# Optimization experiments

Hardware: AMD Instinct MI355X
Metric: run time of the kernel (lower is better)

The kernel has to match this reference:

```python
import jax, jax.numpy as jnp
import numpy as np

H = 1024        # hidden_size
NH = 16         # num_heads
HD = H // NH    # head_dim
DFF = 4 * H
SCALE = HD ** -0.5
EPS = 1e-5


def _ln(x, g, b):
    m = jnp.mean(x, axis=-1, keepdims=True)
    v = jnp.var(x, axis=-1, keepdims=True)
    return (x - m) * jax.lax.rsqrt(v + EPS) * g + b


def _heads(t, B):
    # [B, S, H] -> [B, NH, S, HD]
    return t.reshape(B, -1, NH, HD).transpose(0, 2, 1, 3)


def _merge(t, B):
    # [B, NH, S, HD] -> [B, S, H]
    return t.transpose(0, 2, 1, 3).reshape(B, -1, H)


def _attn(q, k, v):
    s = jnp.einsum('bhqd,bhkd->bhqk', q, k) * SCALE
    p = jax.nn.softmax(s, axis=-1)
    p = jnp.nan_to_num(p, nan=0.0)
    return jnp.einsum('bhqk,bhkd->bhqd', p, v)


def setup_inputs() -> dict:
    key = jax.random.key(0)
    ks = jax.random.split(key, 16)
    std = (2.0 / (5 * H)) ** 0.5
    B, S, SI = 2, 2048, 256
    d = {
        'x': jax.random.normal(ks[0], (B, S, H), jnp.float32),
        'image_features': jax.random.normal(ks[1], (B, SI, H), jnp.float32),
    }
    names = ['sq', 'sk', 'sv', 'so', 'cq', 'ck', 'cv', 'co']
    for i, n in enumerate(names):
        d['W_' + n] = std * jax.random.normal(ks[2 + i], (H, H), jnp.float32)
        d['b_' + n] = jnp.zeros((H,), jnp.float32)
    d['W_ff1'] = std * jax.random.normal(ks[10], (H, DFF), jnp.float32)
    d['b_ff1'] = jnp.zeros((DFF,), jnp.float32)
    d['W_ff2'] = std * jax.random.normal(ks[11], (DFF, H), jnp.float32)
    d['b_ff2'] = jnp.zeros((H,), jnp.float32)
    for n in ['ln1', 'ln2', 'ln3']:
        d['g_' + n] = jnp.ones((H,), jnp.float32)
        d['b_' + n] = jnp.zeros((H,), jnp.float32)
    return d


def reference(x, image_features,
              W_sq, b_sq, W_sk, b_sk, W_sv, b_sv, W_so, b_so,
              W_cq, b_cq, W_ck, b_ck, W_cv, b_cv, W_co, b_co,
              W_ff1, b_ff1, W_ff2, b_ff2,
              g_ln1, b_ln1, g_ln2, b_ln2, g_ln3, b_ln3):
    B = x.shape[0]
    x = x * 0.1
    img = image_features * 0.1

    # --- self attention (pre-norm) ---
    nx = _ln(x, g_ln1, b_ln1)
    q = _heads(nx @ W_sq + b_sq, B)
    k = _heads(nx @ W_sk + b_sk, B)
    v = _heads(nx @ W_sv + b_sv, B)
    so = _merge(_attn(q, k, v), B) @ W_so + b_so
    x = x + so

    # --- cross attention (pre-norm) ---
    nx = _ln(x, g_ln2, b_ln2)
    q = _heads(nx @ W_cq + b_cq, B)
    k = _heads(img @ W_ck + b_ck, B)
    v = _heads(img @ W_cv + b_cv, B)
    co = _merge(_attn(q, k, v), B) @ W_co + b_co
    x = x + co

    # --- feed forward (pre-norm) ---
    nx = _ln(x, g_ln3, b_ln3)
    ff = jax.nn.gelu(nx @ W_ff1 + b_ff1, approximate=False) @ W_ff2 + b_ff2
    x = x + ff
    return x * 10.0
```

## Files before the change

kernel.cpp:

```cpp
#include <hip/hip_runtime.h>
#include <hip/hip_bf16.h>

typedef __bf16 bf16;
typedef __bf16 bf16x4 __attribute__((ext_vector_type(4)));
typedef __bf16 bf16x8 __attribute__((ext_vector_type(8)));
typedef float  f32x4  __attribute__((ext_vector_type(4)));
typedef float  f32x16 __attribute__((ext_vector_type(16)));
typedef int    int4v  __attribute__((ext_vector_type(4)));

#define H_DIM 1024
#define NHEAD 16
#define HD    64
#define QSCL 0.18033688011112042f

__device__ __forceinline__ void gload_lds16(const bf16* g, bf16* l) {
    __builtin_amdgcn_global_load_lds((const __attribute__((address_space(1))) void*)g,
                                     (__attribute__((address_space(3))) void*)l, 16, 0, 0);
}
__device__ __forceinline__ void gload_lds16_u8(const unsigned char* g, unsigned char* l) {
    __builtin_amdgcn_global_load_lds((const __attribute__((address_space(1))) void*)g,
                                     (__attribute__((address_space(3))) void*)l, 16, 0, 0);
}

__device__ __forceinline__ unsigned cvtpk_bf16(float lo, float hi) {
    unsigned r;
    asm volatile("v_cvt_pk_bf16_f32 %0, %1, %2" : "=v"(r) : "v"(lo), "v"(hi));
    return r;
}
__device__ __forceinline__ unsigned cvt2_fp8(float a, float b) {
    unsigned r;
    asm volatile("v_cvt_pk_fp8_f32 %0, %1, %2" : "=v"(r) : "v"(a), "v"(b));
    return r & 0xffffu;
}
__device__ __forceinline__ unsigned pack4_fp8(float a, float b, float c, float d) {
    return cvt2_fp8(a, b) | (cvt2_fp8(c, d) << 16);
}

__device__ __forceinline__ float fexp2(float x) {
    float r;
    asm("v_exp_f32 %0, %1" : "=v"(r) : "v"(x));
    return r;
}

__device__ __forceinline__ void wconv_body(const float* __restrict__ W,
                                           bf16* __restrict__ Wt, int K, int N,
                                           int bx, int by, int t) {
    __shared__ float tile[64][65];
    const int n0 = bx * 64, k0 = by * 64;
#pragma unroll
    for (int p = 0; p < 4; ++p) {
        int lin = p * 1024 + t * 4;
        int r = lin >> 6, c = lin & 63;
        f32x4 v = *(const f32x4*)(W + (size_t)(k0 + r) * N + n0 + c);
        tile[r][c]     = v[0];
        tile[r][c + 1] = v[1];
        tile[r][c + 2] = v[2];
        tile[r][c + 3] = v[3];
    }
    __syncthreads();
#pragma unroll
    for (int p = 0; p < 4; ++p) {
        int lin = p * 1024 + t * 4;
        int rn = lin >> 6, ck = lin & 63;
        bf16x4 o;
#pragma unroll
        for (int j = 0; j < 4; ++j) o[j] = (bf16)tile[ck + j][rn];
        *(bf16x4*)(Wt + (size_t)(n0 + rn) * K + k0 + ck) = o;
    }
}

__global__ __launch_bounds__(256) void wconv_kernel(const float* __restrict__ W,
                                                    bf16* __restrict__ Wt,
                                                    int K, int N) {
    wconv_body(W, Wt, K, N, blockIdx.x, blockIdx.y, threadIdx.x);
}

struct WPtrs { const float* w[4]; bf16* o[4]; };
__global__ __launch_bounds__(256) void wconv4_kernel(WPtrs p) {
    const int m = blockIdx.z;
    wconv_body(p.w[m], p.o[m], 1024, 1024, blockIdx.x, blockIdx.y, threadIdx.x);
}

struct W3Ptrs { const float* w[3]; };
__global__ __launch_bounds__(256) void wconv_fp8_kernel(W3Ptrs p, unsigned char* __restrict__ out) {
    __shared__ float tile[64][65];
    const int m = blockIdx.z, t = threadIdx.x;
    const float* W = p.w[m];
    unsigned char* Wt = out + (size_t)m * 1024 * 1024;
    const int n0 = blockIdx.x * 64, k0 = blockIdx.y * 64;
#pragma unroll
    for (int pp = 0; pp < 4; ++pp) {
        int lin = pp * 1024 + t * 4;
        int r = lin >> 6, c = lin & 63;
        f32x4 v = *(const f32x4*)(W + (size_t)(k0 + r) * 1024 + n0 + c);
        tile[r][c]     = v[0];
        tile[r][c + 1] = v[1];
        tile[r][c + 2] = v[2];
        tile[r][c + 3] = v[3];
    }
    __syncthreads();
#pragma unroll
    for (int pp = 0; pp < 4; ++pp) {
        int lin = pp * 1024 + t * 4;
        int rn = lin >> 6, ck = lin & 63;
        unsigned u = pack4_fp8(tile[ck][rn], tile[ck + 1][rn], tile[ck + 2][rn], tile[ck + 3][rn]);
        *(unsigned*)&Wt[(size_t)(n0 + rn) * 1024 + k0 + ck] = u;
    }
}

__global__ __launch_bounds__(256) void wconv_fp8g(const float* __restrict__ W,
                                                  unsigned char* __restrict__ Wt, int N) {
    __shared__ float tile[64][65];
    const int t = threadIdx.x;
    const int n0 = blockIdx.x * 64, k0 = blockIdx.y * 64;
#pragma unroll
    for (int pp = 0; pp < 4; ++pp) {
        int lin = pp * 1024 + t * 4;
        int r = lin >> 6, c = lin & 63;
        f32x4 v = *(const f32x4*)(W + (size_t)(k0 + r) * N + n0 + c);
        tile[r][c]     = v[0];
        tile[r][c + 1] = v[1];
        tile[r][c + 2] = v[2];
        tile[r][c + 3] = v[3];
    }
    __syncthreads();
#pragma unroll
    for (int pp = 0; pp < 4; ++pp) {
        int lin = pp * 1024 + t * 4;
        int rn = lin >> 6, ck = lin & 63;
        unsigned u = pack4_fp8(tile[ck][rn], tile[ck + 1][rn], tile[ck + 2][rn], tile[ck + 3][rn]);
        *(unsigned*)&Wt[(size_t)(n0 + rn) * 1024 + k0 + ck] = u;
    }
}

__global__ __launch_bounds__(256) void ln_kernel(const float* __restrict__ in, float inScale,
                                                 const float* __restrict__ g,
                                                 const float* __restrict__ b,
                                                 bf16* __restrict__ out) {
    const int row = blockIdx.x, t = threadIdx.x;
    const float* p = in + (size_t)row * H_DIM;
    f32x4 v = *(const f32x4*)(p + t * 4);
    v *= inScale;
    float s1 = v[0] + v[1] + v[2] + v[3];
    float s2 = v[0] * v[0] + v[1] * v[1] + v[2] * v[2] + v[3] * v[3];
#pragma unroll
    for (int m = 1; m < 64; m <<= 1) {
        s1 += __shfl_xor(s1, m);
        s2 += __shfl_xor(s2, m);
    }
    __shared__ float red[8];
    const int wave = t >> 6;
    if ((t & 63) == 0) { red[wave * 2] = s1; red[wave * 2 + 1] = s2; }
    __syncthreads();
    s1 = red[0] + red[2] + red[4] + red[6];
    s2 = red[1] + red[3] + red[5] + red[7];
    float mean = s1 * (1.0f / H_DIM);
    float var  = s2 * (1.0f / H_DIM) - mean * mean;
    float inv  = rsqrtf(var + 1e-5f);
    f32x4 gg = *(const f32x4*)(g + t * 4);
    f32x4 bb = *(const f32x4*)(b + t * 4);
    bf16x4 o;
#pragma unroll
    for (int j = 0; j < 4; ++j) o[j] = (bf16)((v[j] - mean) * inv * gg[j] + bb[j]);
    *(bf16x4*)(out + (size_t)row * H_DIM + t * 4) = o;
}

__global__ __launch_bounds__(256) void ln_fp8_kernel(const float* __restrict__ in, float inScale,
                                                     const float* __restrict__ g,
                                                     const float* __restrict__ b,
                                                     unsigned* __restrict__ out) {
    const int row = blockIdx.x, t = threadIdx.x;
    const float* p = in + (size_t)row * H_DIM;
    f32x4 v = *(const f32x4*)(p + t * 4);
    v *= inScale;
    float s1 = v[0] + v[1] + v[2] + v[3];
    float s2 = v[0] * v[0] + v[1] * v[1] + v[2] * v[2] + v[3] * v[3];
#pragma unroll
    for (int m = 1; m < 64; m <<= 1) {
        s1 += __shfl_xor(s1, m);
        s2 += __shfl_xor(s2, m);
    }
    __shared__ float red[8];
    const int wave = t >> 6;
    if ((t & 63) == 0) { red[wave * 2] = s1; red[wave * 2 + 1] = s2; }
    __syncthreads();
    s1 = red[0] + red[2] + red[4] + red[6];
    s2 = red[1] + red[3] + red[5] + red[7];
    float mean = s1 * (1.0f / H_DIM);
    float var  = s2 * (1.0f / H_DIM) - mean * mean;
    float inv  = rsqrtf(var + 1e-5f);
    f32x4 gg = *(const f32x4*)(g + t * 4);
    f32x4 bb = *(const f32x4*)(b + t * 4);
    float y0 = (v[0] - mean) * inv * gg[0] + bb[0];
    float y1 = (v[1] - mean) * inv * gg[1] + bb[1];
    float y2 = (v[2] - mean) * inv * gg[2] + bb[2];
    float y3 = (v[3] - mean) * inv * gg[3] + bb[3];
    out[row * 256 + t] = pack4_fp8(y0, y1, y2, y3);
}

__global__ __launch_bounds__(256) void cvt_scale_kernel(const float* __restrict__ in,
                                                        bf16* __restrict__ out,
                                                        float s, int n4) {
    int i = blockIdx.x * 256 + threadIdx.x;
    if (i < n4) {
        f32x4 v = *(const f32x4*)(in + (size_t)i * 4);
        bf16x4 o;
#pragma unroll
        for (int j = 0; j < 4; ++j) o[j] = (bf16)(v[j] * s);
        *(bf16x4*)(out + (size_t)i * 4) = o;
    }
}

template <int BM, int BN, int MODE, bool OUT_BF16, bool GELU_EPI, bool HAS_RES>
__global__ __launch_bounds__(256) void gemm_kernel(const bf16* __restrict__ A,
                                                   const bf16* __restrict__ Bt,
                                                   const float* __restrict__ bias1,
                                                   const float* __restrict__ bias2,
                                                   const float* __restrict__ bias3,
                                                   const float* __restrict__ res,
                                                   void* __restrict__ o1, void* __restrict__ o2,
                                                   void* __restrict__ o3,
                                                   int M, int N, int K,
                                                   float resScale, float outScale, int slog2) {
    constexpr int CHUNKS = (BM + BN) / 32;
    constexpr int WRR = BM / 2, WCC = BN / 2;
    constexpr int MI = WRR / 16, NJ = WCC / 16;
    __shared__ bf16 SM[2][(BM + BN) * 64];
    const int nwg = gridDim.x * gridDim.y;
    const int dlin = blockIdx.y * gridDim.x + blockIdx.x;
    const int id = (dlin & 7) * (nwg >> 3) + (dlin >> 3);
    const int bx = id % gridDim.x, by = id / gridDim.x;
    const int m0 = by * BM, n0 = bx * BN;
    const int tid = threadIdx.x;
    const int wave = tid >> 6, lane = tid & 63;
    const int lr = lane & 15, lhi = lane >> 4;
    const int wr = wave >> 1, wc = wave & 1;
    const int sr = lane >> 3, sc8 = (lane & 7) * 8;
    const int sc8x = sc8 ^ (sr << 3);
    const int rxr = (lr & 7) << 3;

    f32x4 acc[MI][NJ] = {};

    auto stage = [&](int buf, int k0) {
#pragma unroll
        for (int p = 0; p < CHUNKS; ++p) {
            const int rr = p * 32 + wave * 8 + sr;
            bf16* l = &SM[buf][0] + p * 2048 + wave * 512;
            const bf16* g = (p < BM / 32)
                ? (A  + (size_t)(m0 + rr) * K + k0 + sc8x)
                : (Bt + (size_t)(n0 + rr - BM) * K + k0 + sc8x);
            gload_lds16(g, l);
        }
    };

    stage(0, 0);
    int buf = 0;
    for (int k0 = 0; k0 < K; k0 += 64) {
        const bool pre = (k0 + 64 < K);
        if (pre) {
            stage(buf ^ 1, k0 + 64);
            asm volatile("s_waitcnt vmcnt(%0)" :: "i"(CHUNKS) : "memory");
        } else {
            asm volatile("s_waitcnt vmcnt(0)" ::: "memory");
        }
        __builtin_amdgcn_sched_barrier(0);
        __builtin_amdgcn_s_barrier();
#pragma unroll
        for (int kk = 0; kk < 2; ++kk) {
            const int sa = (kk * 32 + lhi * 8) ^ rxr;
            bf16x8 af[MI], bfr[NJ];
#pragma unroll
            for (int i = 0; i < MI; ++i)
                af[i] = *(const bf16x8*)&SM[buf][(wr * WRR + i * 16 + lr) * 64 + sa];
#pragma unroll
            for (int j = 0; j < NJ; ++j)
                bfr[j] = *(const bf16x8*)&SM[buf][(BM + wc * WCC + j * 16 + lr) * 64 + sa];
#pragma unroll
            for (int i = 0; i < MI; ++i)
#pragma unroll
                for (int j = 0; j < NJ; ++j)
                    acc[i][j] = __builtin_amdgcn_mfma_f32_16x16x32_bf16(af[i], bfr[j], acc[i][j], 0, 0, 0);
        }
        __builtin_amdgcn_s_barrier();
        buf ^= 1;
    }

#pragma unroll
    for (int i = 0; i < MI; ++i) {
#pragma unroll
        for (int j = 0; j < NJ; ++j) {
            const int col = n0 + wc * WCC + j * 16 + lr;
            const int row0 = m0 + wr * WRR + i * 16 + lhi * 4;
            if (MODE == 0) {
                const float bv = bias1[col];
#pragma unroll
                for (int r = 0; r < 4; ++r) {
                    const int row = row0 + r;
                    const size_t idx = (size_t)row * N + col;
                    float v = acc[i][j][r] + bv;
                    if (HAS_RES) v += res[idx] * resScale;
                    if (GELU_EPI) v = 0.5f * v * (1.0f + erff(v * 0.70710678118654752f));
                    v *= outScale;
                    if (OUT_BF16) ((bf16*)o1)[idx] = (bf16)v;
                    else          ((float*)o1)[idx] = v;
                }
            } else {
                const int sec = col >> 10, cl = col & 1023;
                const bool isV = (sec == 1);
                const float bv = (sec == 0 ? bias1 : bias2)[cl];
                if (!isV) {
                    bf16* dst = (bf16*)o1;
#pragma unroll
                    for (int r = 0; r < 4; ++r)
                        dst[(size_t)(row0 + r) * H_DIM + cl] = (bf16)(acc[i][j][r] + bv);
                } else {
                    bf16* dst = (bf16*)o2;
                    const int S = 1 << slog2;
                    const int hI = cl >> 6, dI = cl & 63;
                    const int bI = row0 >> slog2, s0 = row0 & (S - 1);
                    bf16x4 ov;
#pragma unroll
                    for (int r = 0; r < 4; ++r) ov[r] = (bf16)(acc[i][j][r] + bv);
                    *(bf16x4*)(dst + ((size_t)((bI * NHEAD + hI) * HD + dI)) * S + s0) = ov;
                }
            }
        }
    }
}

__global__ __launch_bounds__(256) void gemm_qkv_fp8(const unsigned char* __restrict__ A8,
                                                    const unsigned char* __restrict__ B8,
                                                    const float* __restrict__ bias1,
                                                    const float* __restrict__ bias2,
                                                    const float* __restrict__ bias3,
                                                    bf16* __restrict__ Qo, bf16* __restrict__ Ko,
                                                    bf16* __restrict__ Vo) {
    constexpr int Kd = 1024;
    __shared__ unsigned char SM[2][256 * 64];
    const int nwg = gridDim.x * gridDim.y;
    const int dlin = blockIdx.y * gridDim.x + blockIdx.x;
    const int id = (dlin & 7) * (nwg >> 3) + (dlin >> 3);
    const int bx = id % gridDim.x, by = id / gridDim.x;
    const int m0 = by * 128, n0 = bx * 128;
    const int tid = threadIdx.x;
    const int wave = tid >> 6, lane = tid & 63;
    const int l31 = lane & 31, l5 = lane >> 5;
    const int wr = wave >> 1, wc = wave & 1;
    const int srow = wave * 16 + (lane >> 2);
    const int sunit = (((lane & 3) ^ ((srow >> 1) & 3)) << 4);
    const int rxc = (l31 >> 1) & 3;

    f32x16 acc[2][2] = {};

    auto stage = [&](int buf, int k0) {
#pragma unroll
        for (int p = 0; p < 4; ++p) {
            const int rr = p * 64 + srow;
            unsigned char* l = &SM[buf][0] + p * 4096 + wave * 1024;
            const unsigned char* g = (p < 2)
                ? (A8 + (size_t)(m0 + rr) * Kd + k0 + sunit)
                : (B8 + (size_t)(n0 + rr - 128) * Kd + k0 + sunit);
            gload_lds16_u8(g, l);
        }
    };

    stage(0, 0);
    int buf = 0;
    for (int k0 = 0; k0 < Kd; k0 += 64) {
        const bool pre = (k0 + 64 < Kd);
        if (pre) {
            stage(buf ^ 1, k0 + 64);
            asm volatile("s_waitcnt vmcnt(4)" ::: "memory");
        } else {
            asm volatile("s_waitcnt vmcnt(0)" ::: "memory");
        }
        __builtin_amdgcn_sched_barrier(0);
        __builtin_amdgcn_s_barrier();
#pragma unroll
        for (int kk = 0; kk < 4; ++kk) {
            const int sa = (((kk ^ rxc) << 4) + l5 * 8);
            long long af[2], bfr[2];
#pragma unroll
            for (int i = 0; i < 2; ++i)
                af[i] = *(const long long*)&SM[buf][(wr * 64 + i * 32 + l31) * 64 + sa];
#pragma unroll
            for (int j = 0; j < 2; ++j)
                bfr[j] = *(const long long*)&SM[buf][(128 + wc * 64 + j * 32 + l31) * 64 + sa];
#pragma unroll
            for (int i = 0; i < 2; ++i)
#pragma unroll
                for (int j = 0; j < 2; ++j)
                    acc[i][j] = __builtin_amdgcn_mfma_f32_32x32x16_fp8_fp8(af[i], bfr[j], acc[i][j], 0, 0, 0);
        }
        __builtin_amdgcn_s_barrier();
        buf ^= 1;
    }

#pragma unroll
    for (int i = 0; i < 2; ++i) {
#pragma unroll
        for (int j = 0; j < 2; ++j) {
            const int col = n0 + wc * 64 + j * 32 + l31;
            const int rbase = m0 + wr * 64 + i * 32 + l5 * 4;
            const int sec = col >> 10, cl = col & 1023;
            const float bv = (sec == 0 ? bias1 : sec == 1 ? bias2 : bias3)[cl];
            if (sec < 2) {
                bf16* dst = (sec == 0) ? Qo : Ko;
                const float sc = (sec == 0) ? QSCL : 1.f;
#pragma unroll
                for (int rq = 0; rq < 4; ++rq)
#pragma unroll
                    for (int rr = 0; rr < 4; ++rr) {
                        const int row = rbase + rq * 8 + rr;
                        dst[(size_t)row * H_DIM + cl] = (bf16)((acc[i][j][rq * 4 + rr] + bv) * sc);
                    }
            } else {
                const int hI = cl >> 6, dI = cl & 63;
#pragma unroll
                for (int rq = 0; rq < 4; ++rq) {
                    const int row0 = rbase + rq * 8;
                    const int bI = row0 >> 11, s0 = row0 & 2047;
                    bf16x4 ov;
#pragma unroll
                    for (int rr = 0; rr < 4; ++rr) ov[rr] = (bf16)(acc[i][j][rq * 4 + rr] + bv);
                    *(bf16x4*)(Vo + ((size_t)((bI * NHEAD + hI) * HD + dI)) * 2048 + s0) = ov;
                }
            }
        }
    }
}

__global__ __launch_bounds__(256) void gemm_f8q(const unsigned char* __restrict__ A8,
                                                const unsigned char* __restrict__ B8,
                                                const float* __restrict__ bias,
                                                bf16* __restrict__ o1, int M, int NOUT) {
    constexpr int Kd = 1024;
    __shared__ unsigned char SM[2][256 * 64];
    const int nwg = gridDim.x * gridDim.y;
    const int dlin = blockIdx.y * gridDim.x + blockIdx.x;
    const int id = (dlin & 7) * (nwg >> 3) + (dlin >> 3);
    const int bx = id % gridDim.x, by = id / gridDim.x;
    const int m0 = by * 128, n0 = bx * 128;
    const int tid = threadIdx.x;
    const int wave = tid >> 6, lane = tid & 63;
    const int l31 = lane & 31, l5 = lane >> 5;
    const int wr = wave >> 1, wc = wave & 1;
    const int srow = wave * 16 + (lane >> 2);
    const int sunit = (((lane & 3) ^ ((srow >> 1) & 3)) << 4);
    const int rxc = (l31 >> 1) & 3;

    f32x16 acc[2][2] = {};

    auto stage = [&](int buf, int k0) {
#pragma unroll
        for (int p = 0; p < 4; ++p) {
            const int rr = p * 64 + srow;
            unsigned char* l = &SM[buf][0] + p * 4096 + wave * 1024;
            const unsigned char* g = (p < 2)
                ? (A8 + (size_t)(m0 + rr) * Kd + k0 + sunit)
                : (B8 + (size_t)(n0 + rr - 128) * Kd + k0 + sunit);
            gload_lds16_u8(g, l);
        }
    };

    stage(0, 0);
    int buf = 0;
    for (int k0 = 0; k0 < Kd; k0 += 64) {
        const bool pre = (k0 + 64 < Kd);
        if (pre) {
            stage(buf ^ 1, k0 + 64);
            asm volatile("s_waitcnt vmcnt(4)" ::: "memory");
        } else {
            asm volatile("s_waitcnt vmcnt(0)" ::: "memory");
        }
        __builtin_amdgcn_sched_barrier(0);
        __builtin_amdgcn_s_barrier();
#pragma unroll
        for (int kk = 0; kk < 4; ++kk) {
            const int sa = (((kk ^ rxc) << 4) + l5 * 8);
            long long af[2], bfr[2];
#pragma unroll
            for (int i = 0; i < 2; ++i)
                af[i] = *(const long long*)&SM[buf][(wr * 64 + i * 32 + l31) * 64 + sa];
#pragma unroll
            for (int j = 0; j < 2; ++j)
                bfr[j] = *(const long long*)&SM[buf][(128 + wc * 64 + j * 32 + l31) * 64 + sa];
#pragma unroll
            for (int i = 0; i < 2; ++i)
#pragma unroll
                for (int j = 0; j < 2; ++j)
                    acc[i][j] = __builtin_amdgcn_mfma_f32_32x32x16_fp8_fp8(af[i], bfr[j], acc[i][j], 0, 0, 0);
        }
        __builtin_amdgcn_s_barrier();
        buf ^= 1;
    }

#pragma unroll
    for (int i = 0; i < 2; ++i) {
#pragma unroll
        for (int j = 0; j < 2; ++j) {
            const int col = n0 + wc * 64 + j * 32 + l31;
            const int rbase = m0 + wr * 64 + i * 32 + l5 * 4;
            const float bv = bias[col];
#pragma unroll
            for (int rq = 0; rq < 4; ++rq)
#pragma unroll
                for (int rr = 0; rr < 4; ++rr) {
                    const int row = rbase + rq * 8 + rr;
                    o1[(size_t)row * NOUT + col] = (bf16)((acc[i][j][rq * 4 + rr] + bv) * QSCL);
                }
        }
    }
}

__global__ __launch_bounds__(256) void attn_kernel(const bf16* __restrict__ Qb,
                                                   const bf16* __restrict__ Kb,
                                                   const bf16* __restrict__ Vt_g,
                                                   bf16* __restrict__ Ob,
                                                   int SQ, int SK) {
    __shared__ bf16 SMEM[2][2][64 * 64];
    const int nwg = gridDim.x * gridDim.y;
    const int dlin = blockIdx.y * gridDim.x + blockIdx.x;
    const int id = (dlin & 7) * (nwg >> 3) + (dlin >> 3);
    const int NQ = gridDim.y;
    const int bh = id / NQ, qt = id - bh * NQ;
    const int b = bh >> 4, h = bh & 15;
    const int q0 = qt * 128;
    const int tid = threadIdx.x, wave = tid >> 6, lane = tid & 63;
    const int lr = lane & 15, lhi = lane >> 4;

    bf16x8 qf[2][2];
#pragma unroll
    for (int qi = 0; qi < 2; ++qi) {
        const bf16* qp = Qb + ((size_t)b * SQ + q0 + wave * 32 + qi * 16 + lr) * H_DIM + h * HD;
        qf[qi][0] = *(const bf16x8*)(qp + lhi * 8);
        qf[qi][1] = *(const bf16x8*)(qp + 32 + lhi * 8);
    }

    const int kx = (((lr & 3) | (((lr >> 2) & 1) << 2)) << 3);
    const int vx = (((lr & 3) | (((lr >> 3) & 1) << 2)) << 3);
    int krow[4];
#pragma unroll
    for (int nf = 0; nf < 4; ++nf)
        krow[nf] = (nf >> 1) * 32 + (lr >> 2) * 8 + (nf & 1) * 4 + (lr & 3);

    const int rS = tid >> 3, cS = (tid & 7) * 8;
    const int kxw = (((rS & 3) | (((rS >> 3) & 1) << 2)) << 3);
    const bf16* Kg = Kb + (size_t)b * SK * H_DIM + h * HD;
    const bf16* Vg = Vt_g + (size_t)bh * 64 * SK;

    bf16x8 onesv;
#pragma unroll
    for (int j = 0; j < 8; ++j) onesv[j] = (bf16)1.0f;

    f32x4 o[2][4] = {};
    f32x4 psum[2] = {};
    bf16x8 gK[2], gV[2];

    auto LOADG = [&](int kb) {
#pragma unroll
        for (int p = 0; p < 2; ++p) {
            gK[p] = *(const bf16x8*)(Kg + (size_t)(kb + p * 32 + rS) * H_DIM + cS);
            gV[p] = *(const bf16x8*)(Vg + (size_t)(p * 32 + rS) * SK + kb + cS);
        }
    };
    auto STORES = [&](int buf) {
#pragma unroll
        for (int p = 0; p < 2; ++p) {
            *(bf16x8*)&SMEM[buf][0][(p * 32 + rS) * 64 + (cS ^ kxw)] = gK[p];
            *(bf16x8*)&SMEM[buf][1][(p * 32 + rS) * 64 + (cS ^ kxw)] = gV[p];
        }
    };
    auto COMPUTE = [&](int buf) {
        f32x4 s[2][4] = {};
        __builtin_amdgcn_s_setprio(1);
#pragma unroll
        for (int nf = 0; nf < 4; ++nf) {
            const int base = krow[nf] * 64;
            bf16x8 kf0 = *(const bf16x8*)&SMEM[buf][0][base + ((lhi * 8) ^ kx)];
            bf16x8 kf1 = *(const bf16x8*)&SMEM[buf][0][base + ((32 + lhi * 8) ^ kx)];
#pragma unroll
            for (int qi = 0; qi < 2; ++qi) {
                s[qi][nf] = __builtin_amdgcn_mfma_f32_16x16x32_bf16(kf0, qf[qi][0], s[qi][nf], 0, 0, 0);
                s[qi][nf] = __builtin_amdgcn_mfma_f32_16x16x32_bf16(kf1, qf[qi][1], s[qi][nf], 0, 0, 0);
            }
        }
        __builtin_amdgcn_s_setprio(0);
        unsigned pw[2][8];
#pragma unroll
        for (int qi = 0; qi < 2; ++qi)
#pragma unroll
            for (int nf = 0; nf < 4; ++nf) {
                float p0 = fexp2(s[qi][nf][0]);
                float p1 = fexp2(s[qi][nf][1]);
                float p2 = fexp2(s[qi][nf][2]);
                float p3 = fexp2(s[qi][nf][3]);
                pw[qi][nf * 2]     = cvtpk_bf16(p0, p1);
                pw[qi][nf * 2 + 1] = cvtpk_bf16(p2, p3);
            }
        __builtin_amdgcn_s_setprio(1);
#pragma unroll
        for (int kk = 0; kk < 2; ++kk) {
            bf16x8 pb[2];
#pragma unroll
            for (int qi = 0; qi < 2; ++qi) {
                int4v w = { (int)pw[qi][kk * 4], (int)pw[qi][kk * 4 + 1],
                            (int)pw[qi][kk * 4 + 2], (int)pw[qi][kk * 4 + 3] };
                pb[qi] = __builtin_bit_cast(bf16x8, w);
                psum[qi] = __builtin_amdgcn_mfma_f32_16x16x32_bf16(onesv, pb[qi], psum[qi], 0, 0, 0);
            }
#pragma unroll
            for (int df = 0; df < 4; ++df) {
                bf16x8 vf = *(const bf16x8*)&SMEM[buf][1][(df * 16 + lr) * 64 + ((kk * 32 + lhi * 8) ^ vx)];
                o[0][df] = __builtin_amdgcn_mfma_f32_16x16x32_bf16(vf, pb[0], o[0][df], 0, 0, 0);
                o[1][df] = __builtin_amdgcn_mfma_f32_16x16x32_bf16(vf, pb[1], o[1][df], 0, 0, 0);
            }
        }
        __builtin_amdgcn_s_setprio(0);
    };

    const int nt = SK >> 6;
    LOADG(0);
    STORES(0);
    if (nt > 1) LOADG(64);
    __syncthreads();
    for (int t = 0; t < nt; ++t) {
        COMPUTE(t & 1);
        if (t + 1 < nt) {
            STORES((t + 1) & 1);
            if (t + 2 < nt) LOADG((t + 2) << 6);
        }
        __syncthreads();
    }

    bf16* T = &SMEM[0][0][0] + wave * (32 * 72);
#pragma unroll
    for (int qi = 0; qi < 2; ++qi) {
        const float inv = 1.0f / psum[qi][0];
#pragma unroll
        for (int df = 0; df < 4; ++df)
#pragma unroll
            for (int r = 0; r < 4; ++r)
                T[(qi * 16 + lr) * 72 + df * 16 + lhi * 4 + r] = (bf16)(o[qi][df][r] * inv);
    }
#pragma unroll
    for (int pp = 0; pp < 4; ++pp) {
        const int r32 = pp * 8 + (lane >> 3), ch = (lane & 7) * 8;
        bf16x8 v = *(const bf16x8*)&T[r32 * 72 + ch];
        *(bf16x8*)(Ob + ((size_t)b * SQ + q0 + wave * 32 + r32) * H_DIM + h * HD + ch) = v;
    }
}

extern "C" void kernel_launch(void* const* d_in, const int* in_sizes, int n_in,
                              void* d_out, int out_size, void* d_ws, size_t ws_size,
                              hipStream_t stream) {
    const float* x    = (const float*)d_in[0];
    const float* img  = (const float*)d_in[1];
    const float* W_sq = (const float*)d_in[2];   const float* b_sq = (const float*)d_in[3];
    const float* W_sk = (const float*)d_in[4];   const float* b_sk = (const float*)d_in[5];
    const float* W_sv = (const float*)d_in[6];   const float* b_sv = (const float*)d_in[7];
    const float* W_so = (const float*)d_in[8];   const float* b_so = (const float*)d_in[9];
    const float* W_cq = (const float*)d_in[10];  const float* b_cq = (const float*)d_in[11];
    const float* W_ck = (const float*)d_in[12];  const float* b_ck = (const float*)d_in[13];
    const float* W_cv = (const float*)d_in[14];  const float* b_cv = (const float*)d_in[15];
    const float* W_co = (const float*)d_in[16];  const float* b_co = (const float*)d_in[17];
    const float* W_f1 = (const float*)d_in[18];  const float* b_f1 = (const float*)d_in[19];
    const float* W_f2 = (const float*)d_in[20];  const float* b_f2 = (const float*)d_in[21];
    const float* g1 = (const float*)d_in[22];    const float* bb1 = (const float*)d_in[23];
    const float* g2 = (const float*)d_in[24];    const float* bb2 = (const float*)d_in[25];
    const float* g3 = (const float*)d_in[26];    const float* bb3 = (const float*)d_in[27];

    char* ws = (char*)d_ws;
    const size_t MB = 1ull << 20;
    unsigned char* LN2_8 = (unsigned char*)(ws + 0 * MB);
    unsigned char* wcq8  = (unsigned char*)(ws + 4 * MB);
    bf16* WT   = (bf16*)ws;
    bf16* w_so = WT + 3 * (1u << 20);
    bf16* w_ck = WT + 5 * (1u << 20);
    bf16* w_cv = WT + 6 * (1u << 20);
    bf16* w_co = WT + 7 * (1u << 20);
    bf16* w_f1 = WT + 8 * (1u << 20);
    bf16* w_f2 = WT + 12 * (1u << 20);
    float* XR  = (float*)(ws + 32 * MB);
    bf16* NX   = (bf16*)(ws + 48 * MB);
    bf16* Qb   = (bf16*)(ws + 56 * MB);
    bf16* Kb   = (bf16*)(ws + 64 * MB);
    bf16* Vt   = (bf16*)(ws + 72 * MB);
    bf16* FF   = (bf16*)(ws + 56 * MB);
    unsigned char* W8  = (unsigned char*)(ws + 80 * MB);
    unsigned char* NX8 = (unsigned char*)(ws + 83 * MB);
    bf16* IMGB = (bf16*)(ws + 88 * MB);

    const dim3 blk(256);

    WPtrs wp;
    wp.w[0] = W_so; wp.o[0] = w_so;  wp.w[1] = W_ck; wp.o[1] = w_ck;
    wp.w[2] = W_cv; wp.o[2] = w_cv;  wp.w[3] = W_co; wp.o[3] = w_co;
    wconv4_kernel<<<dim3(16, 16, 4), blk, 0, stream>>>(wp);
    W3Ptrs w3; w3.w[0] = W_sq; w3.w[1] = W_sk; w3.w[2] = W_sv;
    wconv_fp8_kernel<<<dim3(16, 16, 3), blk, 0, stream>>>(w3, W8);
    wconv_fp8g<<<dim3(16, 16), blk, 0, stream>>>(W_cq, wcq8, 1024);
    wconv_kernel<<<dim3(64, 16), blk, 0, stream>>>(W_f1, w_f1, 1024, 4096);
    wconv_kernel<<<dim3(16, 64), blk, 0, stream>>>(W_f2, w_f2, 4096, 1024);

    ln_fp8_kernel<<<4096, blk, 0, stream>>>(x, 0.1f, g1, bb1, (unsigned*)NX8);
    gemm_qkv_fp8<<<dim3(24, 32), blk, 0, stream>>>(NX8, W8, b_sq, b_sk, b_sv, Qb, Kb, Vt);
    attn_kernel<<<dim3(32, 16), blk, 0, stream>>>(Qb, Kb, Vt, NX, 2048, 2048);
    gemm_kernel<64, 128, 0, false, false, true><<<dim3(8, 64), blk, 0, stream>>>(
        NX, w_so, b_so, nullptr, nullptr, x, XR, nullptr, nullptr, 4096, 1024, 1024, 0.1f, 1.f, 0);

    ln_fp8_kernel<<<4096, blk, 0, stream>>>(XR, 1.f, g2, bb2, (unsigned*)LN2_8);
    gemm_f8q<<<dim3(8, 32), blk, 0, stream>>>(LN2_8, wcq8, b_cq, Qb, 4096, 1024);
    cvt_scale_kernel<<<dim3(512), blk, 0, stream>>>(img, IMGB, 0.1f, 131072);
    gemm_kernel<64, 128, 2, true, false, false><<<dim3(16, 8), blk, 0, stream>>>(
        IMGB, w_ck, b_ck, b_cv, nullptr, nullptr, Kb, Vt, nullptr, 512, 2048, 1024, 0.f, 1.f, 8);
    attn_kernel<<<dim3(32, 16), blk, 0, stream>>>(Qb, Kb, Vt, NX, 2048, 256);
    gemm_kernel<64, 128, 0, false, false, true><<<dim3(8, 64), blk, 0, stream>>>(
        NX, w_co, b_co, nullptr, nullptr, XR, XR, nullptr, nullptr, 4096, 1024, 1024, 1.f, 1.f, 0);

    ln_kernel<<<4096, blk, 0, stream>>>(XR, 1.f, g3, bb3, NX);
    gemm_kernel<128, 128, 0, true, true, false><<<dim3(32, 32), blk, 0, stream>>>(
        NX, w_f1, b_f1, nullptr, nullptr, nullptr, FF, nullptr, nullptr, 4096, 4096, 1024, 0.f, 1.f, 0);
    gemm_kernel<64, 128, 0, false, false, true><<<dim3(8, 64), blk, 0, stream>>>(
        FF, w_f2, b_f2, nullptr, nullptr, XR, d_out, nullptr, nullptr, 4096, 1024, 4096, 1.f, 10.f, 0);
}
```

Baseline: 262.8 us.

## Add 256x256-tile 8-wave FF1 GEMM with phased prefetch and fused GELU

New measurement: 261.8 us. No clear change (-0.4%).

```diff
diff --git a/kernel.cpp b/kernel.cpp
--- a/kernel.cpp
+++ b/kernel.cpp
@@ -35,7 +35,6 @@
 __device__ __forceinline__ unsigned pack4_fp8(float a, float b, float c, float d) {
     return cvt2_fp8(a, b) | (cvt2_fp8(c, d) << 16);
 }
-
 __device__ __forceinline__ float fexp2(float x) {
     float r;
     asm("v_exp_f32 %0, %1" : "=v"(r) : "v"(x));
@@ -328,6 +327,109 @@
     }
 }
 
+__global__ __launch_bounds__(512) void gemm_ff1_8ph(const bf16* __restrict__ A,
+                                                    const bf16* __restrict__ Bt,
+                                                    const float* __restrict__ bias,
+                                                    bf16* __restrict__ out) {
+    extern __shared__ bf16 SM[];
+    constexpr int Kd = 1024, KT = 16;
+    const int nwg = gridDim.x * gridDim.y;
+    const int dlin = blockIdx.y * gridDim.x + blockIdx.x;
+    const int id = (dlin & 7) * (nwg >> 3) + (dlin >> 3);
+    const int bx = id % gridDim.x, by = id / gridDim.x;
+    const int m0 = by * 256, n0 = bx * 256;
+    const int tid = threadIdx.x;
+    const int wave = tid >> 6, lane = tid & 63;
+    const int lr = lane & 15, lhi = lane >> 4;
+    const int wm = wave >> 2, wn = wave & 3;
+    const int rxr = (lr & 7) << 3;
+    const int strow = tid >> 3;
+    const int scol = (((tid & 7) << 3)) ^ (((tid >> 3) & 7) << 3);
+
+    f32x4 acc[8][4] = {};
+
+    auto stageH = [&](int buf, const bf16* gp, int grow0, int kcol0, int region) {
+#pragma unroll
+        for (int s = 0; s < 2; ++s) {
+            bf16* l = &SM[buf * 32768 + region + s * 4096 + wave * 512];
+            gload_lds16(gp + (size_t)(grow0 + s * 64 + strow) * Kd + kcol0 + scol, l);
+        }
+    };
+
+    stageH(0, A, m0, 0, 0);
+    stageH(0, A, m0 + 128, 0, 8192);
+    stageH(0, Bt, n0, 0, 16384);
+    stageH(0, Bt, n0 + 128, 0, 24576);
+    asm volatile("s_waitcnt vmcnt(0)" ::: "memory");
+    __builtin_amdgcn_s_barrier();
+
+    for (int t = 0; t < KT; ++t) {
+        const int buf = t & 1;
+        const int kn = (t + 1) * 64;
+        const bool pre = (t + 1 < KT);
+#pragma unroll
+        for (int p = 0; p < 4; ++p) {
+            const int mh = p >> 1, nh = p & 1;
+            bf16x8 af[4][2], bfr[2][2];
+#pragma unroll
+            for (int kk = 0; kk < 2; ++kk) {
+                const int sa = (kk * 32 + lhi * 8) ^ rxr;
+#pragma unroll
+                for (int i = 0; i < 4; ++i)
+                    af[i][kk] = *(const bf16x8*)&SM[buf * 32768 +
+                        (wm * 128 + mh * 64 + i * 16 + lr) * 64 + sa];
+#pragma unroll
+                for (int j = 0; j < 2; ++j)
+                    bfr[j][kk] = *(const bf16x8*)&SM[buf * 32768 + 16384 +
+                        (wn * 64 + nh * 32 + j * 16 + lr) * 64 + sa];
+            }
+            if (pre) {
+                if (p == 0)      stageH(buf ^ 1, A, m0, kn, 0);
+                else if (p == 1) stageH(buf ^ 1, Bt, n0, kn, 16384);
+                else if (p == 2) stageH(buf ^ 1, Bt, n0 + 128, kn, 24576);
+                else             stageH(buf ^ 1, A, m0 + 128, kn, 8192);
+            }
+            if (pre) {
+                asm volatile("s_waitcnt vmcnt(4)" ::: "memory");
+            } else {
+                if (p == 0)      asm volatile("s_waitcnt vmcnt(2)" ::: "memory");
+                else             asm volatile("s_waitcnt vmcnt(0)" ::: "memory");
+            }
+            __builtin_amdgcn_s_barrier();
+            asm volatile("s_waitcnt lgkmcnt(0)" ::: "memory");
+            __builtin_amdgcn_sched_barrier(0);
+            __builtin_amdgcn_s_setprio(1);
+#pragma unroll
+            for (int i = 0; i < 4; ++i)
+#pragma unroll
+                for (int j = 0; j < 2; ++j) {
+                    acc[mh * 4 + i][nh * 2 + j] = __builtin_amdgcn_mfma_f32_16x16x32_bf16(
+                        af[i][0], bfr[j][0], acc[mh * 4 + i][nh * 2 + j], 0, 0, 0);
+                    acc[mh * 4 + i][nh * 2 + j] = __builtin_amdgcn_mfma_f32_16x16x32_bf16(
+                        af[i][1], bfr[j][1], acc[mh * 4 + i][nh * 2 + j], 0, 0, 0);
+                }
+            __builtin_amdgcn_s_setprio(0);
+            __builtin_amdgcn_s_barrier();
+        }
+    }
+
+#pragma unroll
+    for (int i = 0; i < 8; ++i) {
+#pragma unroll
+        for (int j = 0; j < 4; ++j) {
+            const int col = n0 + wn * 64 + j * 16 + lr;
+            const int row0 = m0 + wm * 128 + i * 16 + lhi * 4;
+            const float bv = bias[col];
+#pragma unroll
+            for (int r = 0; r < 4; ++r) {
+                float v = acc[i][j][r] + bv;
+                v = 0.5f * v * (1.0f + erff(v * 0.70710678118654752f));
+                out[(size_t)(row0 + r) * 4096 + col] = (bf16)v;
+            }
+        }
+    }
+}
+
 __global__ __launch_bounds__(256) void gemm_qkv_fp8(const unsigned char* __restrict__ A8,
                                                     const unsigned char* __restrict__ B8,
                                                     const float* __restrict__ bias1,
@@ -693,6 +795,9 @@
 
     const dim3 blk(256);
 
+    hipFuncSetAttribute((const void*)gemm_ff1_8ph,
+                        hipFuncAttributeMaxDynamicSharedMemorySize, 131072);
+
     WPtrs wp;
     wp.w[0] = W_so; wp.o[0] = w_so;  wp.w[1] = W_ck; wp.o[1] = w_ck;
     wp.w[2] = W_cv; wp.o[2] = w_cv;  wp.w[3] = W_co; wp.o[3] = w_co;
@@ -719,8 +824,7 @@
         NX, w_co, b_co, nullptr, nullptr, XR, XR, nullptr, nullptr, 4096, 1024, 1024, 1.f, 1.f, 0);
 
     ln_kernel<<<4096, blk, 0, stream>>>(XR, 1.f, g3, bb3, NX);
-    gemm_kernel<128, 128, 0, true, true, false><<<dim3(32, 32), blk, 0, stream>>>(
-        NX, w_f1, b_f1, nullptr, nullptr, nullptr, FF, nullptr, nullptr, 4096, 4096, 1024, 0.f, 1.f, 0);
+    gemm_ff1_8ph<<<dim3(16, 16), dim3(512), 131072, stream>>>(NX, w_f1, b_f1, FF);
     gemm_kernel<64, 128, 0, false, false, true><<<dim3(8, 64), blk, 0, stream>>>(
         FF, w_f2, b_f2, nullptr, nullptr, XR, d_out, nullptr, nullptr, 4096, 1024, 4096, 1.f, 10.f, 0);
 }
```
